# Kernel tuning notes

Hardware: AMD Instinct MI355X
Metric: run time of the kernel (lower is better)

The kernel has to match this reference:

```python
import jax, jax.numpy as jnp
import numpy as np

B, C, H, W = 4, 512, 64, 64
C8 = C // 8


def setup_inputs() -> dict:
    key = jax.random.key(0)
    ks = jax.random.split(key, 8)
    return {
        "x": jax.random.normal(ks[0], (B, C, H, W), jnp.float32),
        "wb": jax.random.normal(ks[1], (C8, C), jnp.float32) * 0.05,
        "bb": jax.random.normal(ks[2], (C8,), jnp.float32) * 0.05,
        "wc": jax.random.normal(ks[3], (C8, C), jnp.float32) * 0.05,
        "bc": jax.random.normal(ks[4], (C8,), jnp.float32) * 0.05,
        "wd": jax.random.normal(ks[5], (C, C), jnp.float32) * 0.05,
        "bd": jax.random.normal(ks[6], (C,), jnp.float32) * 0.05,
        "alpha": jax.random.normal(ks[7], (1,), jnp.float32),
    }


def reference(x, wb, bb, wc, bc, wd, bd, alpha):
    b, c, h, w = x.shape
    n = h * w
    xf = x.reshape(b, c, n)  # [B, C, N]
    # 1x1 convs == per-pixel channel matmuls
    feat_b = jnp.einsum('kc,bcn->bkn', wb, xf) + bb[:, None]  # [B, C/8, N]
    feat_c = jnp.einsum('kc,bcn->bkn', wc, xf) + bc[:, None]  # [B, C/8, N]
    # attention_s[n, m] = softmax_m( feat_b[:, n] . feat_c[:, m] )  (no scaling, as in source)
    scores = jnp.einsum('bkn,bkm->bnm', feat_b, feat_c)  # [B, N, N]
    attn = jax.nn.softmax(scores, axis=-1)
    feat_d = jnp.einsum('oc,bcn->bon', wd, xf) + bd[:, None]  # [B, C, N]
    # feat_e = bmm(feat_d, attn^T): fe[c, n] = sum_m fd[c, m] * attn[n, m]
    feat_e = jnp.einsum('bcm,bnm->bcn', feat_d, attn).reshape(b, c, h, w)
    return alpha[0] * feat_e + x
```

## Files before the change

kernel.cpp:

```cpp
#include <hip/hip_runtime.h>
#include <hip/hip_bf16.h>

#define NB 4
#define CC 512
#define CK 64
#define NN 4096

typedef unsigned short u16;
typedef __attribute__((ext_vector_type(8))) __bf16 bf16x8;
typedef __attribute__((ext_vector_type(4))) float f32x4;
typedef __attribute__((ext_vector_type(4))) unsigned int u32x4;
typedef __attribute__((ext_vector_type(8))) unsigned short u16x8;
typedef __attribute__((ext_vector_type(4))) unsigned short u16x4;

__device__ __forceinline__ u16 f2b(float f) {
  union { float f; unsigned u; } x; x.f = f;
  unsigned r = x.u + 0x7fffu + ((x.u >> 16) & 1u);
  return (u16)(r >> 16);
}
__device__ __forceinline__ float b2f(u16 u) {
  union { unsigned u; float f; } x; x.u = ((unsigned)u) << 16; return x.f;
}
__device__ __forceinline__ u16 cvt_bf16(float f) {
  union { __bf16 h; u16 u; } c; c.h = (__bf16)f; return c.u;
}
__device__ __forceinline__ float fast_exp2(float x) {
  float r;
  asm("v_exp_f32 %0, %1" : "=v"(r) : "v"(x));
  return r;
}
__device__ __forceinline__ void lds_barrier() {
  asm volatile("s_waitcnt lgkmcnt(0)" ::: "memory");
  __builtin_amdgcn_s_barrier();
}

#define MFMA16(a, b, c) __builtin_amdgcn_mfma_f32_16x16x32_bf16((a), (b), (c), 0, 0, 0)

__global__ __launch_bounds__(256) void proj_qk(
    const float* __restrict__ x,
    const float* __restrict__ wb, const float* __restrict__ bb,
    const float* __restrict__ wc, const float* __restrict__ bc,
    u16* __restrict__ Qhi, u16* __restrict__ Qlo,
    u16* __restrict__ Khi, u16* __restrict__ Klo)
{
  const int tid = threadIdx.x;
  const int n0 = blockIdx.x * 64;
  const int which = blockIdx.y;
  const int b = blockIdx.z;
  const float* w   = which ? wc : wb;
  const float* bia = which ? bc : bb;
  u16* oh = which ? Khi : Qhi;
  u16* ol = which ? Klo : Qlo;
  const float qsc = which ? 1.0f : 1.44269504088896340736f;

  __shared__ u16 Wh[64][40], Wl[64][40], Xh[64][40], Xl[64][40];

  const int lane = tid & 63, wid = tid >> 6;
  const int wr = wid >> 1, wn = wid & 1;
  const int l15 = lane & 15, lk = (lane >> 4) * 8;

  f32x4 acc[2][2] = {};

  for (int kk = 0; kk < CC; kk += 32) {
    {
      const int row = tid >> 2, c0 = (tid & 3) * 8;
      const float* src = w + (size_t)row * CC + kk + c0;
#pragma unroll
      for (int i = 0; i < 8; ++i) {
        float v = src[i];
        u16 h = f2b(v);
        Wh[row][c0 + i] = h;
        Wl[row][c0 + i] = f2b(v - b2f(h));
      }
    }
    {
      const int cc2 = tid >> 3, j0 = (tid & 7) * 8;
      const float* src = x + ((size_t)b * CC + kk + cc2) * NN + n0 + j0;
#pragma unroll
      for (int i = 0; i < 8; ++i) {
        float v = src[i];
        u16 h = f2b(v);
        Xh[j0 + i][cc2] = h;
        Xl[j0 + i][cc2] = f2b(v - b2f(h));
      }
    }
    __syncthreads();
#pragma unroll
    for (int fi = 0; fi < 2; ++fi) {
      const int ar = wr * 32 + fi * 16 + l15;
      bf16x8 ah = *(const bf16x8*)&Wh[ar][lk];
      bf16x8 al = *(const bf16x8*)&Wl[ar][lk];
#pragma unroll
      for (int fj = 0; fj < 2; ++fj) {
        const int br = wn * 32 + fj * 16 + l15;
        bf16x8 bh = *(const bf16x8*)&Xh[br][lk];
        bf16x8 bl = *(const bf16x8*)&Xl[br][lk];
        acc[fi][fj] = MFMA16(ah, bh, acc[fi][fj]);
        acc[fi][fj] = MFMA16(ah, bl, acc[fi][fj]);
        acc[fi][fj] = MFMA16(al, bh, acc[fi][fj]);
      }
    }
    __syncthreads();
  }

#pragma unroll
  for (int fi = 0; fi < 2; ++fi) {
    const int d0 = wr * 32 + fi * 16 + (lane >> 4) * 4;
#pragma unroll
    for (int fj = 0; fj < 2; ++fj) {
      const int n = n0 + wn * 32 + fj * 16 + l15;
      u16x4 vh, vl;
#pragma unroll
      for (int r = 0; r < 4; ++r) {
        float v = (acc[fi][fj][r] + bia[d0 + r]) * qsc;
        u16 h = f2b(v);
        vh[r] = h;
        vl[r] = f2b(v - b2f(h));
      }
      *(u16x4*)&oh[((size_t)b * NN + n) * CK + d0] = vh;
      *(u16x4*)&ol[((size_t)b * NN + n) * CK + d0] = vl;
    }
  }
}

__global__ __launch_bounds__(256) void proj_v(
    const float* __restrict__ x,
    const float* __restrict__ wd, const float* __restrict__ bd,
    u16* __restrict__ Vt)
{
  const int tid = threadIdx.x;
  const int n0 = blockIdx.x * 64;
  const int o0 = blockIdx.y * 64;
  const int b = blockIdx.z;

  __shared__ u16 Wt[64][40], Xt[64][40];
  const int lane = tid & 63, wid = tid >> 6;
  const int wr = wid >> 1, wn = wid & 1;
  const int l15 = lane & 15, lk = (lane >> 4) * 8;

  f32x4 acc[2][2] = {};
  for (int kk = 0; kk < CC; kk += 32) {
    {
      const int row = tid >> 2, c0 = (tid & 3) * 8;
      const float* src = wd + (size_t)(o0 + row) * CC + kk + c0;
#pragma unroll
      for (int i = 0; i < 8; ++i) Wt[row][c0 + i] = f2b(src[i]);
    }
    {
      const int cc2 = tid >> 3, j0 = (tid & 7) * 8;
      const float* src = x + ((size_t)b * CC + kk + cc2) * NN + n0 + j0;
#pragma unroll
      for (int i = 0; i < 8; ++i) Xt[j0 + i][cc2] = f2b(src[i]);
    }
    __syncthreads();
#pragma unroll
    for (int fi = 0; fi < 2; ++fi) {
      bf16x8 a = *(const bf16x8*)&Wt[wr * 32 + fi * 16 + l15][lk];
#pragma unroll
      for (int fj = 0; fj < 2; ++fj) {
        bf16x8 bv = *(const bf16x8*)&Xt[wn * 32 + fj * 16 + l15][lk];
        acc[fi][fj] = MFMA16(a, bv, acc[fi][fj]);
      }
    }
    __syncthreads();
  }
#pragma unroll
  for (int fi = 0; fi < 2; ++fi) {
    const int d0 = o0 + wr * 32 + fi * 16 + (lane >> 4) * 4;
#pragma unroll
    for (int fj = 0; fj < 2; ++fj) {
      const int n = n0 + wn * 32 + fj * 16 + l15;
#pragma unroll
      for (int r = 0; r < 4; ++r)
        Vt[((size_t)b * CC + d0 + r) * NN + n] = f2b(acc[fi][fj][r] + bd[d0 + r]);
    }
  }
}

struct alignas(16) AttnLds {
  u16 kh[64][64];
  u16 kl[64][64];
  float s[64][68];
  u16 p[64][64];
  float m[64];
  float l[64];
  float sc[64];
};

__global__ __launch_bounds__(256, 2) void attn(
    const u16* __restrict__ Qhi, const u16* __restrict__ Qlo,
    const u16* __restrict__ Khi, const u16* __restrict__ Klo,
    const u16* __restrict__ Vt,
    const float* __restrict__ x, const float* __restrict__ alpha,
    float* __restrict__ out)
{
  __shared__ AttnLds L;
  const int tid = threadIdx.x;
  const int lane = tid & 63, wid = tid >> 6;
  const int bid = blockIdx.x;
  const int b = (bid >> 1) & 3;
  const int qt = bid >> 3;
  const int ohalf = bid & 1;
  const int q0 = qt * 64;
  const int l15 = lane & 15;
  const int lk8 = (lane >> 4) * 8;

  const int srow = tid >> 2;
  const int sch  = (tid & 3) * 16;
  const int ssw0 = sch ^ ((srow & 7) << 3);
  const int ssw1 = (sch + 8) ^ ((srow & 7) << 3);

  bf16x8 qah[2], qal[2];
  {
    const size_t qg = ((size_t)b * NN + q0 + wid * 16 + l15) * CK + lk8;
    qah[0] = *(const bf16x8*)&Qhi[qg];
    qah[1] = *(const bf16x8*)&Qhi[qg + 32];
    qal[0] = *(const bf16x8*)&Qlo[qg];
    qal[1] = *(const bf16x8*)&Qlo[qg + 32];
  }
  {
    const size_t g = ((size_t)b * NN + srow) * CK + sch;
    *(u32x4*)&L.kh[srow][ssw0] = *(const u32x4*)&Khi[g];
    *(u32x4*)&L.kh[srow][ssw1] = *(const u32x4*)&Khi[g + 8];
    *(u32x4*)&L.kl[srow][ssw0] = *(const u32x4*)&Klo[g];
    *(u32x4*)&L.kl[srow][ssw1] = *(const u32x4*)&Klo[g + 8];
  }
  if (tid < 64) { L.m[tid] = -__builtin_huge_valf(); L.l[tid] = 0.f; }

  const u16* vbase = Vt + ((size_t)b * CC + ohalf * 256 + wid * 64 + l15) * NN + lk8;

  f32x4 accO[4][4] = {};

  __syncthreads();

  for (int t = 0; t < 64; ++t) {
    const int m0 = t * 64;
    const bool hasNext = (t < 63);

    u32x4 kh0, kh1, kl0, kl1;
    if (hasNext) {
      const size_t g = ((size_t)b * NN + m0 + 64 + srow) * CK + sch;
      kh0 = *(const u32x4*)&Khi[g];
      kh1 = *(const u32x4*)&Khi[g + 8];
      kl0 = *(const u32x4*)&Klo[g];
      kl1 = *(const u32x4*)&Klo[g + 8];
    }
    bf16x8 vr[2][4];
#pragma unroll
    for (int f_ = 0; f_ < 4; ++f_)
#pragma unroll
      for (int ks = 0; ks < 2; ++ks)
        vr[ks][f_] = *(const bf16x8*)(vbase + (size_t)f_ * 16 * NN + m0 + ks * 32);

    __builtin_amdgcn_s_setprio(1);
#pragma unroll
    for (int fj = 0; fj < 4; ++fj) {
      f32x4 s = {};
#pragma unroll
      for (int ks = 0; ks < 2; ++ks) {
        const int k = ks * 32 + lk8;
        const int br = fj * 16 + l15;
        bf16x8 bh = *(const bf16x8*)&L.kh[br][k ^ ((br & 7) << 3)];
        bf16x8 bl = *(const bf16x8*)&L.kl[br][k ^ ((br & 7) << 3)];
        s = MFMA16(qah[ks], bh, s);
        s = MFMA16(qah[ks], bl, s);
        s = MFMA16(qal[ks], bh, s);
      }
      const int r0 = wid * 16 + (lane >> 4) * 4, c0 = fj * 16 + l15;
#pragma unroll
      for (int r = 0; r < 4; ++r) L.s[r0 + r][c0] = s[r];
    }
    __builtin_amdgcn_s_setprio(0);
    lds_barrier();

    if (hasNext) {
      *(u32x4*)&L.kh[srow][ssw0] = kh0;
      *(u32x4*)&L.kh[srow][ssw1] = kh1;
      *(u32x4*)&L.kl[srow][ssw0] = kl0;
      *(u32x4*)&L.kl[srow][ssw1] = kl1;
    }
    {
      const int row = srow, sub = tid & 3;
      const float* sr = &L.s[row][sch];
      f32x4 a0 = *(const f32x4*)&sr[0];
      f32x4 a1 = *(const f32x4*)&sr[4];
      f32x4 a2 = *(const f32x4*)&sr[8];
      f32x4 a3 = *(const f32x4*)&sr[12];
      float mx = fmaxf(fmaxf(fmaxf(a0[0], a0[1]), fmaxf(a0[2], a0[3])),
                       fmaxf(fmaxf(a1[0], a1[1]), fmaxf(a1[2], a1[3])));
      mx = fmaxf(mx, fmaxf(fmaxf(fmaxf(a2[0], a2[1]), fmaxf(a2[2], a2[3])),
                           fmaxf(fmaxf(a3[0], a3[1]), fmaxf(a3[2], a3[3]))));
      mx = fmaxf(mx, __shfl_xor(mx, 1));
      mx = fmaxf(mx, __shfl_xor(mx, 2));
      const float mOld = L.m[row];
      const bool grow = (mx > mOld + 11.5f);
      const float mNew = grow ? mx : mOld;
      float pv[16];
      float sum = 0.f;
#pragma unroll
      for (int j = 0; j < 4; ++j) { pv[j]      = fast_exp2(a0[j] - mNew); sum += pv[j]; }
#pragma unroll
      for (int j = 0; j < 4; ++j) { pv[4 + j]  = fast_exp2(a1[j] - mNew); sum += pv[4 + j]; }
#pragma unroll
      for (int j = 0; j < 4; ++j) { pv[8 + j]  = fast_exp2(a2[j] - mNew); sum += pv[8 + j]; }
#pragma unroll
      for (int j = 0; j < 4; ++j) { pv[12 + j] = fast_exp2(a3[j] - mNew); sum += pv[12 + j]; }
      sum += __shfl_xor(sum, 1);
      sum += __shfl_xor(sum, 2);
      const float scf = grow ? fast_exp2(mOld - mNew) : 1.0f;
      if (sub == 0) {
        if (grow) L.m[row] = mNew;
        L.l[row] = L.l[row] * scf + sum;
        L.sc[row] = scf;
      }
      u16x8 pb0, pb1;
#pragma unroll
      for (int j = 0; j < 8; ++j) pb0[j] = cvt_bf16(pv[j]);
#pragma unroll
      for (int j = 0; j < 8; ++j) pb1[j] = cvt_bf16(pv[8 + j]);
      *(u16x8*)&L.p[row][ssw0] = pb0;
      *(u16x8*)&L.p[row][ssw1] = pb1;
    }
    lds_barrier();

    {
      f32x4 scv[4];
      bool need = false;
#pragma unroll
      for (int f_ = 0; f_ < 4; ++f_) {
        scv[f_] = *(const f32x4*)&L.sc[f_ * 16 + (lane >> 4) * 4];
        need |= (scv[f_][0] != 1.0f) | (scv[f_][1] != 1.0f) |
                (scv[f_][2] != 1.0f) | (scv[f_][3] != 1.0f);
      }
      if (__any(need)) {
#pragma unroll
        for (int f_ = 0; f_ < 4; ++f_)
#pragma unroll
          for (int fj = 0; fj < 4; ++fj)
#pragma unroll
            for (int r = 0; r < 4; ++r)
              accO[f_][fj][r] *= scv[f_][r];
      }
    }
    __builtin_amdgcn_s_setprio(1);
#pragma unroll
    for (int ks = 0; ks < 2; ++ks) {
      const int k = ks * 32 + lk8;
      bf16x8 a[4];
#pragma unroll
      for (int f_ = 0; f_ < 4; ++f_) {
        const int ar = f_ * 16 + l15;
        a[f_] = *(const bf16x8*)&L.p[ar][k ^ ((ar & 7) << 3)];
      }
#pragma unroll
      for (int fj = 0; fj < 4; ++fj)
#pragma unroll
        for (int f_ = 0; f_ < 4; ++f_)
          accO[f_][fj] = MFMA16(a[f_], vr[ks][fj], accO[f_][fj]);
    }
    __builtin_amdgcn_s_setprio(0);
  }
  __syncthreads();
  const float al = alpha[0];
#pragma unroll
  for (int f_ = 0; f_ < 4; ++f_) {
    const int r0 = f_ * 16 + (lane >> 4) * 4;
    const float rl0 = 1.f / L.l[r0],     rl1 = 1.f / L.l[r0 + 1];
    const float rl2 = 1.f / L.l[r0 + 2], rl3 = 1.f / L.l[r0 + 3];
    const int n_ = q0 + r0;
#pragma unroll
    for (int fj = 0; fj < 4; ++fj) {
      const int c_ = ohalf * 256 + wid * 64 + fj * 16 + l15;
      const size_t g = ((size_t)b * CC + c_) * NN + n_;
      f32x4 xv = *(const f32x4*)&x[g];
      f32x4 ov;
      ov[0] = fmaf(al, accO[f_][fj][0] * rl0, xv[0]);
      ov[1] = fmaf(al, accO[f_][fj][1] * rl1, xv[1]);
      ov[2] = fmaf(al, accO[f_][fj][2] * rl2, xv[2]);
      ov[3] = fmaf(al, accO[f_][fj][3] * rl3, xv[3]);
      *(f32x4*)&out[g] = ov;
    }
  }
}

extern "C" void kernel_launch(void* const* d_in, const int* in_sizes, int n_in,
                              void* d_out, int out_size, void* d_ws, size_t ws_size,
                              hipStream_t stream) {
  const float* x     = (const float*)d_in[0];
  const float* wb    = (const float*)d_in[1];
  const float* bb    = (const float*)d_in[2];
  const float* wc    = (const float*)d_in[3];
  const float* bc    = (const float*)d_in[4];
  const float* wd    = (const float*)d_in[5];
  const float* bd    = (const float*)d_in[6];
  const float* alpha = (const float*)d_in[7];
  float* out = (float*)d_out;

  u16* Qhi = (u16*)d_ws;
  u16* Qlo = Qhi + (size_t)NB * NN * CK;
  u16* Khi = Qlo + (size_t)NB * NN * CK;
  u16* Klo = Khi + (size_t)NB * NN * CK;
  u16* Vt  = Klo + (size_t)NB * NN * CK;

  proj_qk<<<dim3(NN / 64, 2, NB), 256, 0, stream>>>(x, wb, bb, wc, bc, Qhi, Qlo, Khi, Klo);
  proj_v<<<dim3(NN / 64, CC / 64, NB), 256, 0, stream>>>(x, wd, bd, Vt);
  attn<<<dim3(512), 256, 0, stream>>>(Qhi, Qlo, Khi, Klo, Vt, x, alpha, out);
}
```

Baseline: 231.5 us.

## Software-pipeline attention loop: overlap PV MFMA of previous tile with softmax

Double-buffers the P tile and rescale factors in LDS and carries the V registers across iterations. The PV matrix multiply for tile t-1 now runs in iteration t, between the QK MFMA phase and the softmax of tile t, and a final epilogue finishes the last tile. The goal is to overlap MFMA work with softmax VALU work and to hide V load latency behind a whole iteration, while removing one barrier-bounded phase. In exchange it uses more LDS and more registers (an extra set of V fragments), which could cause spills or lower occupancy under launch_bounds(256,2).

```diff
diff --git a/kernel.cpp b/kernel.cpp
--- a/kernel.cpp
+++ b/kernel.cpp
@@ -181,10 +181,10 @@
   u16 kh[64][64];
   u16 kl[64][64];
   float s[64][68];
-  u16 p[64][64];
+  u16 p[2][64][64];
   float m[64];
   float l[64];
-  float sc[64];
+  float sc[2][64];
 };
 
 __global__ __launch_bounds__(256, 2) void attn(
@@ -230,12 +230,15 @@
   const u16* vbase = Vt + ((size_t)b * CC + ohalf * 256 + wid * 64 + l15) * NN + lk8;
 
   f32x4 accO[4][4] = {};
+  bf16x8 vp0[4], vp1[4];
 
   __syncthreads();
 
+#pragma unroll 2
   for (int t = 0; t < 64; ++t) {
     const int m0 = t * 64;
     const bool hasNext = (t < 63);
+    const int cur = t & 1, prev = cur ^ 1;
 
     u32x4 kh0, kh1, kl0, kl1;
     if (hasNext) {
@@ -245,12 +248,12 @@
       kl0 = *(const u32x4*)&Klo[g];
       kl1 = *(const u32x4*)&Klo[g + 8];
     }
-    bf16x8 vr[2][4];
-#pragma unroll
-    for (int f_ = 0; f_ < 4; ++f_)
-#pragma unroll
-      for (int ks = 0; ks < 2; ++ks)
-        vr[ks][f_] = *(const bf16x8*)(vbase + (size_t)f_ * 16 * NN + m0 + ks * 32);
+    bf16x8 vn0[4], vn1[4];
+#pragma unroll
+    for (int f_ = 0; f_ < 4; ++f_) {
+      vn0[f_] = *(const bf16x8*)(vbase + (size_t)f_ * 16 * NN + m0);
+      vn1[f_] = *(const bf16x8*)(vbase + (size_t)f_ * 16 * NN + m0 + 32);
+    }
 
     __builtin_amdgcn_s_setprio(1);
 #pragma unroll
@@ -279,6 +282,44 @@
       *(u32x4*)&L.kl[srow][ssw0] = kl0;
       *(u32x4*)&L.kl[srow][ssw1] = kl1;
     }
+
+    if (t > 0) {
+      f32x4 scv[4];
+      bool need = false;
+#pragma unroll
+      for (int f_ = 0; f_ < 4; ++f_) {
+        scv[f_] = *(const f32x4*)&L.sc[prev][f_ * 16 + (lane >> 4) * 4];
+        need |= (scv[f_][0] != 1.0f) | (scv[f_][1] != 1.0f) |
+                (scv[f_][2] != 1.0f) | (scv[f_][3] != 1.0f);
+      }
+      if (__any(need)) {
+#pragma unroll
+        for (int f_ = 0; f_ < 4; ++f_)
+#pragma unroll
+          for (int fj = 0; fj < 4; ++fj)
+#pragma unroll
+            for (int r = 0; r < 4; ++r)
+              accO[f_][fj][r] *= scv[f_][r];
+      }
+      __builtin_amdgcn_s_setprio(1);
+#pragma unroll
+      for (int ks = 0; ks < 2; ++ks) {
+        const int k = ks * 32 + lk8;
+        bf16x8 a[4];
+#pragma unroll
+        for (int f_ = 0; f_ < 4; ++f_) {
+          const int ar = f_ * 16 + l15;
+          a[f_] = *(const bf16x8*)&L.p[prev][ar][k ^ ((ar & 7) << 3)];
+        }
+#pragma unroll
+        for (int fj = 0; fj < 4; ++fj)
+#pragma unroll
+          for (int f_ = 0; f_ < 4; ++f_)
+            accO[f_][fj] = MFMA16(a[f_], ks ? vp1[fj] : vp0[fj], accO[f_][fj]);
+      }
+      __builtin_amdgcn_s_setprio(0);
+    }
+
     {
       const int row = srow, sub = tid & 3;
       const float* sr = &L.s[row][sch];
@@ -311,38 +352,40 @@
       if (sub == 0) {
         if (grow) L.m[row] = mNew;
         L.l[row] = L.l[row] * scf + sum;
-        L.sc[row] = scf;
+        L.sc[cur][row] = scf;
       }
       u16x8 pb0, pb1;
 #pragma unroll
       for (int j = 0; j < 8; ++j) pb0[j] = cvt_bf16(pv[j]);
 #pragma unroll
       for (int j = 0; j < 8; ++j) pb1[j] = cvt_bf16(pv[8 + j]);
-      *(u16x8*)&L.p[row][ssw0] = pb0;
-      *(u16x8*)&L.p[row][ssw1] = pb1;
+      *(u16x8*)&L.p[cur][row][ssw0] = pb0;
+      *(u16x8*)&L.p[cur][row][ssw1] = pb1;
     }
     lds_barrier();
 
-    {
-      f32x4 scv[4];
-      bool need = false;
-#pragma unroll
-      for (int f_ = 0; f_ < 4; ++f_) {
-        scv[f_] = *(const f32x4*)&L.sc[f_ * 16 + (lane >> 4) * 4];
-        need |= (scv[f_][0] != 1.0f) | (scv[f_][1] != 1.0f) |
-                (scv[f_][2] != 1.0f) | (scv[f_][3] != 1.0f);
-      }
-      if (__any(need)) {
-#pragma unroll
-        for (int f_ = 0; f_ < 4; ++f_)
-#pragma unroll
-          for (int fj = 0; fj < 4; ++fj)
-#pragma unroll
-            for (int r = 0; r < 4; ++r)
-              accO[f_][fj][r] *= scv[f_][r];
-      }
-    }
-    __builtin_amdgcn_s_setprio(1);
+#pragma unroll
+    for (int f_ = 0; f_ < 4; ++f_) { vp0[f_] = vn0[f_]; vp1[f_] = vn1[f_]; }
+  }
+
+  {
+    f32x4 scv[4];
+    bool need = false;
+#pragma unroll
+    for (int f_ = 0; f_ < 4; ++f_) {
+      scv[f_] = *(const f32x4*)&L.sc[1][f_ * 16 + (lane >> 4) * 4];
+      need |= (scv[f_][0] != 1.0f) | (scv[f_][1] != 1.0f) |
+              (scv[f_][2] != 1.0f) | (scv[f_][3] != 1.0f);
+    }
+    if (__any(need)) {
+#pragma unroll
+      for (int f_ = 0; f_ < 4; ++f_)
+#pragma unroll
+        for (int fj = 0; fj < 4; ++fj)
+#pragma unroll
+          for (int r = 0; r < 4; ++r)
+            accO[f_][fj][r] *= scv[f_][r];
+    }
 #pragma unroll
     for (int ks = 0; ks < 2; ++ks) {
       const int k = ks * 32 + lk8;
@@ -350,15 +393,14 @@
 #pragma unroll
       for (int f_ = 0; f_ < 4; ++f_) {
         const int ar = f_ * 16 + l15;
-        a[f_] = *(const bf16x8*)&L.p[ar][k ^ ((ar & 7) << 3)];
+        a[f_] = *(const bf16x8*)&L.p[1][ar][k ^ ((ar & 7) << 3)];
       }
 #pragma unroll
       for (int fj = 0; fj < 4; ++fj)
 #pragma unroll
         for (int f_ = 0; f_ < 4; ++f_)
-          accO[f_][fj] = MFMA16(a[f_], vr[ks][fj], accO[f_][fj]);
-    }
-    __builtin_amdgcn_s_setprio(0);
+          accO[f_][fj] = MFMA16(a[f_], ks ? vp1[fj] : vp0[fj], accO[f_][fj]);
+    }
   }
   __syncthreads();
   const float al = alpha[0];
```

Result: no change. 232.5 us (+0.4%).

## Halve attention query tile to 32 rows and double grid for occupancy

Applied to the files above, without the earlier changes.

The attention kernel now handles 32 query rows per block instead of 64, doubling the grid to 1024 blocks and raising launch bounds to 4 blocks per CU. The score computation is redistributed so each wave computes one query fragment against two key fragments, and the softmax uses 8 threads per row. This shrinks LDS and accumulator registers to allow more resident blocks and better latency hiding. The cost is that K and V tiles are loaded and V is streamed twice as often per query, raising global and LDS traffic per unit of work.

```diff
diff --git a/kernel.cpp b/kernel.cpp
--- a/kernel.cpp
+++ b/kernel.cpp
@@ -180,14 +180,14 @@
 struct alignas(16) AttnLds {
   u16 kh[64][64];
   u16 kl[64][64];
-  float s[64][68];
-  u16 p[64][64];
-  float m[64];
-  float l[64];
-  float sc[64];
+  float s[32][68];
+  u16 p[32][64];
+  float m[32];
+  float l[32];
+  float sc[32];
 };
 
-__global__ __launch_bounds__(256, 2) void attn(
+__global__ __launch_bounds__(256, 4) void attn(
     const u16* __restrict__ Qhi, const u16* __restrict__ Qlo,
     const u16* __restrict__ Khi, const u16* __restrict__ Klo,
     const u16* __restrict__ Vt,
@@ -201,22 +201,29 @@
   const int b = (bid >> 1) & 3;
   const int qt = bid >> 3;
   const int ohalf = bid & 1;
-  const int q0 = qt * 64;
+  const int q0 = qt * 32;
   const int l15 = lane & 15;
   const int lk8 = (lane >> 4) * 8;
+
+  const int qf = wid >> 1;
+  const int kf0 = (wid & 1) * 2;
 
   const int srow = tid >> 2;
   const int sch  = (tid & 3) * 16;
   const int ssw0 = sch ^ ((srow & 7) << 3);
   const int ssw1 = (sch + 8) ^ ((srow & 7) << 3);
 
-  bf16x8 qah[2], qal[2];
-  {
-    const size_t qg = ((size_t)b * NN + q0 + wid * 16 + l15) * CK + lk8;
-    qah[0] = *(const bf16x8*)&Qhi[qg];
-    qah[1] = *(const bf16x8*)&Qhi[qg + 32];
-    qal[0] = *(const bf16x8*)&Qlo[qg];
-    qal[1] = *(const bf16x8*)&Qlo[qg + 32];
+  const int xrow = tid >> 3, xsub = tid & 7;
+  const int xsw = (xsub * 8) ^ ((xrow & 7) << 3);
+
+  bf16x8 qah[2][2], qal[2][2];
+#pragma unroll
+  for (int f_ = 0; f_ < 2; ++f_) {
+    const size_t qg = ((size_t)b * NN + q0 + f_ * 16 + l15) * CK + lk8;
+    qah[f_][0] = *(const bf16x8*)&Qhi[qg];
+    qah[f_][1] = *(const bf16x8*)&Qhi[qg + 32];
+    qal[f_][0] = *(const bf16x8*)&Qlo[qg];
+    qal[f_][1] = *(const bf16x8*)&Qlo[qg + 32];
   }
   {
     const size_t g = ((size_t)b * NN + srow) * CK + sch;
@@ -225,11 +232,11 @@
     *(u32x4*)&L.kl[srow][ssw0] = *(const u32x4*)&Klo[g];
     *(u32x4*)&L.kl[srow][ssw1] = *(const u32x4*)&Klo[g + 8];
   }
-  if (tid < 64) { L.m[tid] = -__builtin_huge_valf(); L.l[tid] = 0.f; }
+  if (tid < 32) { L.m[tid] = -__builtin_huge_valf(); L.l[tid] = 0.f; }
 
   const u16* vbase = Vt + ((size_t)b * CC + ohalf * 256 + wid * 64 + l15) * NN + lk8;
 
-  f32x4 accO[4][4] = {};
+  f32x4 accO[2][4] = {};
 
   __syncthreads();
 
@@ -254,19 +261,20 @@
 
     __builtin_amdgcn_s_setprio(1);
 #pragma unroll
-    for (int fj = 0; fj < 4; ++fj) {
+    for (int f2 = 0; f2 < 2; ++f2) {
+      const int kf = kf0 + f2;
       f32x4 s = {};
 #pragma unroll
       for (int ks = 0; ks < 2; ++ks) {
         const int k = ks * 32 + lk8;
-        const int br = fj * 16 + l15;
+        const int br = kf * 16 + l15;
         bf16x8 bh = *(const bf16x8*)&L.kh[br][k ^ ((br & 7) << 3)];
         bf16x8 bl = *(const bf16x8*)&L.kl[br][k ^ ((br & 7) << 3)];
-        s = MFMA16(qah[ks], bh, s);
-        s = MFMA16(qah[ks], bl, s);
-        s = MFMA16(qal[ks], bh, s);
-      }
-      const int r0 = wid * 16 + (lane >> 4) * 4, c0 = fj * 16 + l15;
+        s = MFMA16(qah[qf][ks], bh, s);
+        s = MFMA16(qah[qf][ks], bl, s);
+        s = MFMA16(qal[qf][ks], bh, s);
+      }
+      const int r0 = qf * 16 + (lane >> 4) * 4, c0 = kf * 16 + l15;
 #pragma unroll
       for (int r = 0; r < 4; ++r) L.s[r0 + r][c0] = s[r];
     }
@@ -280,61 +288,51 @@
       *(u32x4*)&L.kl[srow][ssw1] = kl1;
     }
     {
-      const int row = srow, sub = tid & 3;
-      const float* sr = &L.s[row][sch];
+      const float* sr = &L.s[xrow][xsub * 8];
       f32x4 a0 = *(const f32x4*)&sr[0];
       f32x4 a1 = *(const f32x4*)&sr[4];
-      f32x4 a2 = *(const f32x4*)&sr[8];
-      f32x4 a3 = *(const f32x4*)&sr[12];
       float mx = fmaxf(fmaxf(fmaxf(a0[0], a0[1]), fmaxf(a0[2], a0[3])),
                        fmaxf(fmaxf(a1[0], a1[1]), fmaxf(a1[2], a1[3])));
-      mx = fmaxf(mx, fmaxf(fmaxf(fmaxf(a2[0], a2[1]), fmaxf(a2[2], a2[3])),
-                           fmaxf(fmaxf(a3[0], a3[1]), fmaxf(a3[2], a3[3]))));
       mx = fmaxf(mx, __shfl_xor(mx, 1));
       mx = fmaxf(mx, __shfl_xor(mx, 2));
-      const float mOld = L.m[row];
+      mx = fmaxf(mx, __shfl_xor(mx, 4));
+      const float mOld = L.m[xrow];
       const bool grow = (mx > mOld + 11.5f);
       const float mNew = grow ? mx : mOld;
-      float pv[16];
+      float pv[8];
       float sum = 0.f;
 #pragma unroll
-      for (int j = 0; j < 4; ++j) { pv[j]      = fast_exp2(a0[j] - mNew); sum += pv[j]; }
-#pragma unroll
-      for (int j = 0; j < 4; ++j) { pv[4 + j]  = fast_exp2(a1[j] - mNew); sum += pv[4 + j]; }
-#pragma unroll
-      for (int j = 0; j < 4; ++j) { pv[8 + j]  = fast_exp2(a2[j] - mNew); sum += pv[8 + j]; }
-#pragma unroll
-      for (int j = 0; j < 4; ++j) { pv[12 + j] = fast_exp2(a3[j] - mNew); sum += pv[12 + j]; }
+      for (int j = 0; j < 4; ++j) { pv[j]     = fast_exp2(a0[j] - mNew); sum += pv[j]; }
+#pragma unroll
+      for (int j = 0; j < 4; ++j) { pv[4 + j] = fast_exp2(a1[j] - mNew); sum += pv[4 + j]; }
       sum += __shfl_xor(sum, 1);
       sum += __shfl_xor(sum, 2);
+      sum += __shfl_xor(sum, 4);
       const float scf = grow ? fast_exp2(mOld - mNew) : 1.0f;
-      if (sub == 0) {
-        if (grow) L.m[row] = mNew;
-        L.l[row] = L.l[row] * scf + sum;
-        L.sc[row] = scf;
-      }
-      u16x8 pb0, pb1;
-#pragma unroll
-      for (int j = 0; j < 8; ++j) pb0[j] = cvt_bf16(pv[j]);
-#pragma unroll
-      for (int j = 0; j < 8; ++j) pb1[j] = cvt_bf16(pv[8 + j]);
-      *(u16x8*)&L.p[row][ssw0] = pb0;
-      *(u16x8*)&L.p[row][ssw1] = pb1;
+      if (xsub == 0) {
+        if (grow) L.m[xrow] = mNew;
+        L.l[xrow] = L.l[xrow] * scf + sum;
+        L.sc[xrow] = scf;
+      }
+      u16x8 pb;
+#pragma unroll
+      for (int j = 0; j < 8; ++j) pb[j] = cvt_bf16(pv[j]);
+      *(u16x8*)&L.p[xrow][xsw] = pb;
     }
     lds_barrier();
 
     {
-      f32x4 scv[4];
+      f32x4 scv[2];
       bool need = false;
 #pragma unroll
-      for (int f_ = 0; f_ < 4; ++f_) {
+      for (int f_ = 0; f_ < 2; ++f_) {
         scv[f_] = *(const f32x4*)&L.sc[f_ * 16 + (lane >> 4) * 4];
         need |= (scv[f_][0] != 1.0f) | (scv[f_][1] != 1.0f) |
                 (scv[f_][2] != 1.0f) | (scv[f_][3] != 1.0f);
       }
       if (__any(need)) {
 #pragma unroll
-        for (int f_ = 0; f_ < 4; ++f_)
+        for (int f_ = 0; f_ < 2; ++f_)
 #pragma unroll
           for (int fj = 0; fj < 4; ++fj)
 #pragma unroll
@@ -346,16 +344,16 @@
 #pragma unroll
     for (int ks = 0; ks < 2; ++ks) {
       const int k = ks * 32 + lk8;
-      bf16x8 a[4];
-#pragma unroll
-      for (int f_ = 0; f_ < 4; ++f_) {
+      bf16x8 a[2];
+#pragma unroll
+      for (int f_ = 0; f_ < 2; ++f_) {
         const int ar = f_ * 16 + l15;
         a[f_] = *(const bf16x8*)&L.p[ar][k ^ ((ar & 7) << 3)];
       }
 #pragma unroll
       for (int fj = 0; fj < 4; ++fj)
 #pragma unroll
-        for (int f_ = 0; f_ < 4; ++f_)
+        for (int f_ = 0; f_ < 2; ++f_)
           accO[f_][fj] = MFMA16(a[f_], vr[ks][fj], accO[f_][fj]);
     }
     __builtin_amdgcn_s_setprio(0);
@@ -363,7 +361,7 @@
   __syncthreads();
   const float al = alpha[0];
 #pragma unroll
-  for (int f_ = 0; f_ < 4; ++f_) {
+  for (int f_ = 0; f_ < 2; ++f_) {
     const int r0 = f_ * 16 + (lane >> 4) * 4;
     const float rl0 = 1.f / L.l[r0],     rl1 = 1.f / L.l[r0 + 1];
     const float rl2 = 1.f / L.l[r0 + 2], rl3 = 1.f / L.l[r0 + 3];
@@ -404,5 +402,5 @@
 
   proj_qk<<<dim3(NN / 64, 2, NB), 256, 0, stream>>>(x, wb, bb, wc, bc, Qhi, Qlo, Khi, Klo);
   proj_v<<<dim3(NN / 64, CC / 64, NB), 256, 0, stream>>>(x, wd, bd, Vt);
-  attn<<<dim3(512), 256, 0, stream>>>(Qhi, Qlo, Khi, Klo, Vt, x, alpha, out);
-}
+  attn<<<dim3(1024), 256, 0, stream>>>(Qhi, Qlo, Khi, Klo, Vt, x, alpha, out);
+}
```

After: 437.4 us. 88.9% more time.

## Keep softmax in registers via transposed QK^T and double-buffer K and P tiles

Applied to the files above, without the earlier changes.

The score MFMA is transposed (K as A operand, Q as B) so each lane holds a full query row's scores across lane groups. This lets the row max and sum be done with cross-lane shuffles and kept in registers, with no fp32 score tile staged through LDS. K, P and the rescale factors are double-buffered so one barrier per iteration is removed. Launch bounds drop the minimum of two blocks per CU, which may change register allocation and occupancy.

```diff
diff --git a/kernel.cpp b/kernel.cpp
--- a/kernel.cpp
+++ b/kernel.cpp
@@ -178,16 +178,14 @@
 }
 
 struct alignas(16) AttnLds {
-  u16 kh[64][64];
-  u16 kl[64][64];
-  float s[64][68];
-  u16 p[64][64];
-  float m[64];
+  u16 kh[2][64][64];
+  u16 kl[2][64][64];
+  u16 p[2][64][64];
+  float sc[2][64];
   float l[64];
-  float sc[64];
 };
 
-__global__ __launch_bounds__(256, 2) void attn(
+__global__ __launch_bounds__(256) void attn(
     const u16* __restrict__ Qhi, const u16* __restrict__ Qlo,
     const u16* __restrict__ Khi, const u16* __restrict__ Klo,
     const u16* __restrict__ Vt,
@@ -203,29 +201,34 @@
   const int ohalf = bid & 1;
   const int q0 = qt * 64;
   const int l15 = lane & 15;
-  const int lk8 = (lane >> 4) * 8;
+  const int g = lane >> 4;
+  const int lk8 = g * 8;
+  const int psw = (l15 & 7) << 3;
 
   const int srow = tid >> 2;
   const int sch  = (tid & 3) * 16;
   const int ssw0 = sch ^ ((srow & 7) << 3);
   const int ssw1 = (sch + 8) ^ ((srow & 7) << 3);
 
-  bf16x8 qah[2], qal[2];
+  bf16x8 qah0, qah1, qal0, qal1;
   {
     const size_t qg = ((size_t)b * NN + q0 + wid * 16 + l15) * CK + lk8;
-    qah[0] = *(const bf16x8*)&Qhi[qg];
-    qah[1] = *(const bf16x8*)&Qhi[qg + 32];
-    qal[0] = *(const bf16x8*)&Qlo[qg];
-    qal[1] = *(const bf16x8*)&Qlo[qg + 32];
+    qah0 = *(const bf16x8*)&Qhi[qg];
+    qah1 = *(const bf16x8*)&Qhi[qg + 32];
+    qal0 = *(const bf16x8*)&Qlo[qg];
+    qal1 = *(const bf16x8*)&Qlo[qg + 32];
   }
   {
-    const size_t g = ((size_t)b * NN + srow) * CK + sch;
-    *(u32x4*)&L.kh[srow][ssw0] = *(const u32x4*)&Khi[g];
-    *(u32x4*)&L.kh[srow][ssw1] = *(const u32x4*)&Khi[g + 8];
-    *(u32x4*)&L.kl[srow][ssw0] = *(const u32x4*)&Klo[g];
-    *(u32x4*)&L.kl[srow][ssw1] = *(const u32x4*)&Klo[g + 8];
-  }
-  if (tid < 64) { L.m[tid] = -__builtin_huge_valf(); L.l[tid] = 0.f; }
+    const size_t gK = ((size_t)b * NN + srow) * CK + sch;
+    *(u32x4*)&L.kh[0][srow][ssw0] = *(const u32x4*)&Khi[gK];
+    *(u32x4*)&L.kh[0][srow][ssw1] = *(const u32x4*)&Khi[gK + 8];
+    *(u32x4*)&L.kl[0][srow][ssw0] = *(const u32x4*)&Klo[gK];
+    *(u32x4*)&L.kl[0][srow][ssw1] = *(const u32x4*)&Klo[gK + 8];
+  }
+
+  float m_reg = -__builtin_huge_valf();
+  float l_reg = 0.f;
+  const int qrow = wid * 16 + l15;
 
   const u16* vbase = Vt + ((size_t)b * CC + ohalf * 256 + wid * 64 + l15) * NN + lk8;
 
@@ -236,14 +239,15 @@
   for (int t = 0; t < 64; ++t) {
     const int m0 = t * 64;
     const bool hasNext = (t < 63);
+    const int cur = t & 1;
 
     u32x4 kh0, kh1, kl0, kl1;
     if (hasNext) {
-      const size_t g = ((size_t)b * NN + m0 + 64 + srow) * CK + sch;
-      kh0 = *(const u32x4*)&Khi[g];
-      kh1 = *(const u32x4*)&Khi[g + 8];
-      kl0 = *(const u32x4*)&Klo[g];
-      kl1 = *(const u32x4*)&Klo[g + 8];
+      const size_t gK = ((size_t)b * NN + m0 + 64 + srow) * CK + sch;
+      kh0 = *(const u32x4*)&Khi[gK];
+      kh1 = *(const u32x4*)&Khi[gK + 8];
+      kl0 = *(const u32x4*)&Klo[gK];
+      kl1 = *(const u32x4*)&Klo[gK + 8];
     }
     bf16x8 vr[2][4];
 #pragma unroll
@@ -252,74 +256,79 @@
       for (int ks = 0; ks < 2; ++ks)
         vr[ks][f_] = *(const bf16x8*)(vbase + (size_t)f_ * 16 * NN + m0 + ks * 32);
 
+    f32x4 sf0, sf1, sf2, sf3;
     __builtin_amdgcn_s_setprio(1);
-#pragma unroll
-    for (int fj = 0; fj < 4; ++fj) {
-      f32x4 s = {};
-#pragma unroll
-      for (int ks = 0; ks < 2; ++ks) {
-        const int k = ks * 32 + lk8;
-        const int br = fj * 16 + l15;
-        bf16x8 bh = *(const bf16x8*)&L.kh[br][k ^ ((br & 7) << 3)];
-        bf16x8 bl = *(const bf16x8*)&L.kl[br][k ^ ((br & 7) << 3)];
-        s = MFMA16(qah[ks], bh, s);
-        s = MFMA16(qah[ks], bl, s);
-        s = MFMA16(qal[ks], bh, s);
-      }
-      const int r0 = wid * 16 + (lane >> 4) * 4, c0 = fj * 16 + l15;
-#pragma unroll
-      for (int r = 0; r < 4; ++r) L.s[r0 + r][c0] = s[r];
+    {
+#define QKT_KF(SF, KF)                                                       \
+      {                                                                      \
+        const int br = (KF) * 16 + l15;                                      \
+        const int ksw = (br & 7) << 3;                                       \
+        bf16x8 kh_0 = *(const bf16x8*)&L.kh[cur][br][lk8 ^ ksw];             \
+        bf16x8 kl_0 = *(const bf16x8*)&L.kl[cur][br][lk8 ^ ksw];             \
+        bf16x8 kh_1 = *(const bf16x8*)&L.kh[cur][br][(32 + lk8) ^ ksw];      \
+        bf16x8 kl_1 = *(const bf16x8*)&L.kl[cur][br][(32 + lk8) ^ ksw];      \
+        f32x4 s_ = {};                                                       \
+        s_ = MFMA16(kh_0, qah0, s_);                                         \
+        s_ = MFMA16(kh_0, qal0, s_);                                         \
+        s_ = MFMA16(kl_0, qah0, s_);                                         \
+        s_ = MFMA16(kh_1, qah1, s_);                                         \
+        s_ = MFMA16(kh_1, qal1, s_);                                         \
+        s_ = MFMA16(kl_1, qah1, s_);                                         \
+        SF = s_;                                                             \
+      }
+      QKT_KF(sf0, 0)
+      QKT_KF(sf1, 1)
+      QKT_KF(sf2, 2)
+      QKT_KF(sf3, 3)
+#undef QKT_KF
     }
     __builtin_amdgcn_s_setprio(0);
-    lds_barrier();
-
+
+    {
+      float mx = fmaxf(
+          fmaxf(fmaxf(fmaxf(sf0[0], sf0[1]), fmaxf(sf0[2], sf0[3])),
+                fmaxf(fmaxf(sf1[0], sf1[1]), fmaxf(sf1[2], sf1[3]))),
+          fmaxf(fmaxf(fmaxf(sf2[0], sf2[1]), fmaxf(sf2[2], sf2[3])),
+                fmaxf(fmaxf(sf3[0], sf3[1]), fmaxf(sf3[2], sf3[3]))));
+      mx = fmaxf(mx, __shfl_xor(mx, 16));
+      mx = fmaxf(mx, __shfl_xor(mx, 32));
+      const bool grow = (mx > m_reg + 11.5f);
+      const float mNew = grow ? mx : m_reg;
+      f32x4 e0, e1, e2, e3;
+      float sum = 0.f;
+#pragma unroll
+      for (int r = 0; r < 4; ++r) { e0[r] = fast_exp2(sf0[r] - mNew); sum += e0[r]; }
+#pragma unroll
+      for (int r = 0; r < 4; ++r) { e1[r] = fast_exp2(sf1[r] - mNew); sum += e1[r]; }
+#pragma unroll
+      for (int r = 0; r < 4; ++r) { e2[r] = fast_exp2(sf2[r] - mNew); sum += e2[r]; }
+#pragma unroll
+      for (int r = 0; r < 4; ++r) { e3[r] = fast_exp2(sf3[r] - mNew); sum += e3[r]; }
+      sum += __shfl_xor(sum, 16);
+      sum += __shfl_xor(sum, 32);
+      const float scf = grow ? fast_exp2(m_reg - mNew) : 1.0f;
+      m_reg = mNew;
+      l_reg = l_reg * scf + sum;
+      if (g == 0) L.sc[cur][qrow] = scf;
+      u16x4 pb;
+#pragma unroll
+      for (int r = 0; r < 4; ++r) pb[r] = cvt_bf16(e0[r]);
+      *(u16x4*)&L.p[cur][qrow][(0 * 16 + g * 4) ^ psw] = pb;
+#pragma unroll
+      for (int r = 0; r < 4; ++r) pb[r] = cvt_bf16(e1[r]);
+      *(u16x4*)&L.p[cur][qrow][(1 * 16 + g * 4) ^ psw] = pb;
+#pragma unroll
+      for (int r = 0; r < 4; ++r) pb[r] = cvt_bf16(e2[r]);
+      *(u16x4*)&L.p[cur][qrow][(2 * 16 + g * 4) ^ psw] = pb;
+#pragma unroll
+      for (int r = 0; r < 4; ++r) pb[r] = cvt_bf16(e3[r]);
+      *(u16x4*)&L.p[cur][qrow][(3 * 16 + g * 4) ^ psw] = pb;
+    }
     if (hasNext) {
-      *(u32x4*)&L.kh[srow][ssw0] = kh0;
-      *(u32x4*)&L.kh[srow][ssw1] = kh1;
-      *(u32x4*)&L.kl[srow][ssw0] = kl0;
-      *(u32x4*)&L.kl[srow][ssw1] = kl1;
-    }
-    {
-      const int row = srow, sub = tid & 3;
-      const float* sr = &L.s[row][sch];
-      f32x4 a0 = *(const f32x4*)&sr[0];
-      f32x4 a1 = *(const f32x4*)&sr[4];
-      f32x4 a2 = *(const f32x4*)&sr[8];
-      f32x4 a3 = *(const f32x4*)&sr[12];
-      float mx = fmaxf(fmaxf(fmaxf(a0[0], a0[1]), fmaxf(a0[2], a0[3])),
-                       fmaxf(fmaxf(a1[0], a1[1]), fmaxf(a1[2], a1[3])));
-      mx = fmaxf(mx, fmaxf(fmaxf(fmaxf(a2[0], a2[1]), fmaxf(a2[2], a2[3])),
-                           fmaxf(fmaxf(a3[0], a3[1]), fmaxf(a3[2], a3[3]))));
-      mx = fmaxf(mx, __shfl_xor(mx, 1));
-      mx = fmaxf(mx, __shfl_xor(mx, 2));
-      const float mOld = L.m[row];
-      const bool grow = (mx > mOld + 11.5f);
-      const float mNew = grow ? mx : mOld;
-      float pv[16];
-      float sum = 0.f;
-#pragma unroll
-      for (int j = 0; j < 4; ++j) { pv[j]      = fast_exp2(a0[j] - mNew); sum += pv[j]; }
-#pragma unroll
-      for (int j = 0; j < 4; ++j) { pv[4 + j]  = fast_exp2(a1[j] - mNew); sum += pv[4 + j]; }
-#pragma unroll
-      for (int j = 0; j < 4; ++j) { pv[8 + j]  = fast_exp2(a2[j] - mNew); sum += pv[8 + j]; }
-#pragma unroll
-      for (int j = 0; j < 4; ++j) { pv[12 + j] = fast_exp2(a3[j] - mNew); sum += pv[12 + j]; }
-      sum += __shfl_xor(sum, 1);
-      sum += __shfl_xor(sum, 2);
-      const float scf = grow ? fast_exp2(mOld - mNew) : 1.0f;
-      if (sub == 0) {
-        if (grow) L.m[row] = mNew;
-        L.l[row] = L.l[row] * scf + sum;
-        L.sc[row] = scf;
-      }
-      u16x8 pb0, pb1;
-#pragma unroll
-      for (int j = 0; j < 8; ++j) pb0[j] = cvt_bf16(pv[j]);
-#pragma unroll
-      for (int j = 0; j < 8; ++j) pb1[j] = cvt_bf16(pv[8 + j]);
-      *(u16x8*)&L.p[row][ssw0] = pb0;
-      *(u16x8*)&L.p[row][ssw1] = pb1;
+      *(u32x4*)&L.kh[cur ^ 1][srow][ssw0] = kh0;
+      *(u32x4*)&L.kh[cur ^ 1][srow][ssw1] = kh1;
+      *(u32x4*)&L.kl[cur ^ 1][srow][ssw0] = kl0;
+      *(u32x4*)&L.kl[cur ^ 1][srow][ssw1] = kl1;
     }
     lds_barrier();
 
@@ -328,7 +337,7 @@
       bool need = false;
 #pragma unroll
       for (int f_ = 0; f_ < 4; ++f_) {
-        scv[f_] = *(const f32x4*)&L.sc[f_ * 16 + (lane >> 4) * 4];
+        scv[f_] = *(const f32x4*)&L.sc[cur][f_ * 16 + g * 4];
         need |= (scv[f_][0] != 1.0f) | (scv[f_][1] != 1.0f) |
                 (scv[f_][2] != 1.0f) | (scv[f_][3] != 1.0f);
       }
@@ -350,7 +359,7 @@
 #pragma unroll
       for (int f_ = 0; f_ < 4; ++f_) {
         const int ar = f_ * 16 + l15;
-        a[f_] = *(const bf16x8*)&L.p[ar][k ^ ((ar & 7) << 3)];
+        a[f_] = *(const bf16x8*)&L.p[cur][ar][k ^ ((ar & 7) << 3)];
       }
 #pragma unroll
       for (int fj = 0; fj < 4; ++fj)
@@ -360,25 +369,26 @@
     }
     __builtin_amdgcn_s_setprio(0);
   }
+  if (g == 0) L.l[qrow] = l_reg;
   __syncthreads();
   const float al = alpha[0];
 #pragma unroll
   for (int f_ = 0; f_ < 4; ++f_) {
-    const int r0 = f_ * 16 + (lane >> 4) * 4;
+    const int r0 = f_ * 16 + g * 4;
     const float rl0 = 1.f / L.l[r0],     rl1 = 1.f / L.l[r0 + 1];
     const float rl2 = 1.f / L.l[r0 + 2], rl3 = 1.f / L.l[r0 + 3];
     const int n_ = q0 + r0;
 #pragma unroll
     for (int fj = 0; fj < 4; ++fj) {
       const int c_ = ohalf * 256 + wid * 64 + fj * 16 + l15;
-      const size_t g = ((size_t)b * CC + c_) * NN + n_;
-      f32x4 xv = *(const f32x4*)&x[g];
+      const size_t gG = ((size_t)b * CC + c_) * NN + n_;
+      f32x4 xv = *(const f32x4*)&x[gG];
       f32x4 ov;
       ov[0] = fmaf(al, accO[f_][fj][0] * rl0, xv[0]);
       ov[1] = fmaf(al, accO[f_][fj][1] * rl1, xv[1]);
       ov[2] = fmaf(al, accO[f_][fj][2] * rl2, xv[2]);
       ov[3] = fmaf(al, accO[f_][fj][3] * rl3, xv[3]);
-      *(f32x4*)&out[g] = ov;
+      *(f32x4*)&out[gG] = ov;
     }
   }
 }
```

Result: slower. 326.8 us (+41.2%).
